# Kernel tuning notes

Hardware: AMD Instinct MI355X
Metric: run time of the kernel (lower is better)

The kernel has to match this reference:

```python
import jax, jax.numpy as jnp
import numpy as np

B, T, E, H, D = 1, 2048, 1024, 16, 64  # H*D == E required by module


def setup_inputs() -> dict:
    key = jax.random.key(0)
    ks = jax.random.split(key, 9)
    s_in = (2.0 / E) ** 0.5
    return {
        "x": jax.random.normal(ks[0], (B, T, E), jnp.float32),
        "wq": jax.random.normal(ks[1], (H * D, E), jnp.float32) * E ** -0.5,
        "wk": jax.random.normal(ks[2], (H * D, E), jnp.float32) * E ** -0.5,
        "wv": jax.random.normal(ks[3], (H * D, E), jnp.float32) * E ** -0.5,
        "wr": jax.random.normal(ks[4], (H, E, T), jnp.float32) * s_in,
        "wvr": jax.random.normal(ks[5], (H * D, E), jnp.float32) * E ** -0.5,
        "wj": jax.random.normal(ks[6], (E, E), jnp.float32) * E ** -0.5,
        "gate": jnp.zeros((H, 3), jnp.float32),
        "wo": jax.random.normal(ks[7], (E, H * D), jnp.float32) * E ** -0.5,
    }


def reference(x, wq, wk, wv, wr, wvr, wj, gate, wo):
    Bx, Tx, Ex = x.shape
    Hh = wr.shape[0]
    Dd = wq.shape[0] // Hh
    scale = 1.0 / Dd ** 0.5
    neg = -jnp.inf
    mask = jnp.triu(jnp.ones((Tx, Tx), bool), 1)  # True above diagonal

    def heads(w):  # (B,T,H*D) -> (B,H,T,D)
        return (x @ w.T).reshape(Bx, Tx, Hh, Dd).transpose(0, 2, 1, 3)

    # --- branch 1: standard causal QKV attention ---
    q, k, v = heads(wq), heads(wk), heads(wv)
    qkv_attn = jnp.einsum('bhqd,bhkd->bhqk', q, k) * scale
    qkv_attn = jnp.where(mask, neg, qkv_attn)
    qkv_out = jnp.einsum('bhqk,bhkd->bhqd', jax.nn.softmax(qkv_attn, axis=-1), v)

    # --- branch 2: RRPRAM learned per-position scores ---
    rv = heads(wvr)
    r = jnp.einsum('bte,het->bht', x, wr[:, :, :Tx])  # (B,H,T) key scores
    r_attn = jnp.where(mask, neg, (r * scale)[:, :, None, :])  # (B,H,T,T)
    rrp_out = jnp.einsum('bhqk,bhkd->bhqd', jax.nn.softmax(r_attn, axis=-1), rv)

    # --- branch 3: Janus self-resonance ---
    echo = x @ wj.T            # (B,T,E)
    echo_back = echo @ wj      # F.linear(echo, wj.weight.T)
    scores = (x * echo_back).sum(-1) / Ex ** 0.5  # (B,T)
    j_attn = jnp.where(mask, neg, scores[:, :, None] * scores[:, None, :])  # (B,T,T)
    jA = jax.nn.softmax(j_attn, axis=-1)
    j_val = echo.reshape(Bx, Tx, Hh, Dd).transpose(0, 2, 1, 3)
    jan_out = jnp.einsum('bqk,bhkd->bhqd', jA, j_val)

    # --- gated combine + output proj ---
    g = jax.nn.softmax(gate, axis=-1)  # (H,3)
    out = (g[:, 0][None, :, None, None] * qkv_out
           + g[:, 1][None, :, None, None] * rrp_out
           + g[:, 2][None, :, None, None] * jan_out)
    out = out.transpose(0, 2, 1, 3).reshape(Bx, Tx, Hh * Dd)
    return out @ wo.T
```

## Files before the change

kernel.cpp:

```cpp
#include <hip/hip_runtime.h>
#include <cstddef>
#include <cstdint>

#define TT 2048
#define EE 1024
#define HH 16

typedef unsigned short ushort;
typedef unsigned int uint;
typedef __attribute__((ext_vector_type(8))) short short8;
typedef __attribute__((ext_vector_type(8))) _Float16 half8;
typedef __attribute__((ext_vector_type(4))) float f32x4;
typedef __attribute__((ext_vector_type(4))) ushort ushort4v;

__device__ __forceinline__ ushort f2bf(float f) {
  uint u = __builtin_bit_cast(uint, f);
  u = (u + 0x7FFFu + ((u >> 16) & 1u)) >> 16;
  return (ushort)u;
}
__device__ __forceinline__ float bf2f(ushort h) {
  return __builtin_bit_cast(float, (uint)h << 16);
}
__device__ __forceinline__ ushort f2h(float f) {
  return __builtin_bit_cast(ushort, (_Float16)f);
}

__device__ __forceinline__ void async16(ushort* lds, const ushort* g) {
  __builtin_amdgcn_global_load_lds(
      reinterpret_cast<const __attribute__((address_space(1))) void*>(
          reinterpret_cast<uintptr_t>(g)),
      reinterpret_cast<__attribute__((address_space(3))) void*>(
          static_cast<unsigned int>(reinterpret_cast<uintptr_t>(lds))),
      16, 0, 0);
}

__global__ __launch_bounds__(256) void cvt_all(
    const float* __restrict__ x, ushort* __restrict__ xbf,
    ushort* __restrict__ xh, ushort* __restrict__ xTbf,
    const float* __restrict__ w0, const float* __restrict__ w1,
    const float* __restrict__ w2, const float* __restrict__ w3,
    const float* __restrict__ w4, const float* __restrict__ w5,
    ushort* __restrict__ d0, ushort* __restrict__ d1,
    ushort* __restrict__ d2, ushort* __restrict__ d3,
    ushort* __restrict__ d4, ushort* __restrict__ d5,
    float* __restrict__ snorm)
{
  const int z = blockIdx.z;
  if (z == 0) {
    __shared__ float tile[32][33];
    if (blockIdx.x == 0 && blockIdx.y == 0) {
      for (int i = threadIdx.x; i < TT; i += 256) snorm[i] = 0.f;
    }
    const int bn = blockIdx.x * 32;
    const int bm = blockIdx.y * 32;
    const int c4 = (threadIdx.x & 7) * 4;
    const int r  = threadIdx.x >> 3;
    const size_t off = (size_t)(bm + r) * EE + bn + c4;
    float4 v = *(const float4*)(x + off);
    tile[r][c4 + 0] = v.x; tile[r][c4 + 1] = v.y;
    tile[r][c4 + 2] = v.z; tile[r][c4 + 3] = v.w;
    ushort4v b, h;
    b.x = f2bf(v.x); b.y = f2bf(v.y); b.z = f2bf(v.z); b.w = f2bf(v.w);
    h.x = f2h(v.x);  h.y = f2h(v.y);  h.z = f2h(v.z);  h.w = f2h(v.w);
    *(ushort4v*)(xbf + off) = b;
    *(ushort4v*)(xh + off) = h;
    __syncthreads();
    const int t4 = (threadIdx.x & 7) * 4;
    const int e  = threadIdx.x >> 3;
    ushort4v tb;
    tb.x = f2bf(tile[t4 + 0][e]); tb.y = f2bf(tile[t4 + 1][e]);
    tb.z = f2bf(tile[t4 + 2][e]); tb.w = f2bf(tile[t4 + 3][e]);
    *(ushort4v*)(xTbf + (size_t)(bn + e) * TT + bm + t4) = tb;
    return;
  }
  const int lin = blockIdx.y * 32 + blockIdx.x;
  if (lin >= 1024) return;
  const float* src; ushort* dst;
  switch (z) {
    case 1: src = w0; dst = d0; break;
    case 2: src = w1; dst = d1; break;
    case 3: src = w2; dst = d2; break;
    case 4: src = w3; dst = d3; break;
    case 5: src = w4; dst = d4; break;
    default: src = w5; dst = d5; break;
  }
  const int i = lin * 1024 + threadIdx.x * 4;
  float4 v = *(const float4*)(src + i);
  ushort4v o;
  if (z == 6) {
    o.x = f2h(v.x); o.y = f2h(v.y); o.z = f2h(v.z); o.w = f2h(v.w);
  } else {
    o.x = f2bf(v.x); o.y = f2bf(v.y); o.z = f2bf(v.z); o.w = f2bf(v.w);
  }
  *(ushort4v*)(dst + i) = o;
}

__global__ __launch_bounds__(256) void proj5(
    const ushort* __restrict__ Abf, const ushort* __restrict__ Ah,
    const ushort* __restrict__ B0, const ushort* __restrict__ B1,
    const ushort* __restrict__ B2, const ushort* __restrict__ B3,
    const ushort* __restrict__ B4,
    ushort* __restrict__ C0, ushort* __restrict__ C1,
    ushort* __restrict__ C2, ushort* __restrict__ C3,
    ushort* __restrict__ C4, float* __restrict__ snorm,
    int M, int N, int K)
{
  const ushort* A; const ushort* B; ushort* C; int om;
  switch (blockIdx.z) {
    case 0: A = Abf; B = B0; C = C0; om = 1; break;
    case 1: A = Abf; B = B1; C = C1; om = 1; break;
    case 2: A = Abf; B = B2; C = C2; om = 2; break;
    case 3: A = Abf; B = B3; C = C3; om = 1; break;
    default: A = Ah; B = B4; C = C4; om = 3; break;
  }
  const bool f16 = (blockIdx.z == 4);
  __shared__ __align__(16) ushort As[2][128 * 64];
  __shared__ __align__(16) ushort Bs[2][128 * 64];
  const int tid = threadIdx.x;
  const int m0 = blockIdx.y * 128, n0 = blockIdx.x * 128;
  const int w = tid >> 6, lane = tid & 63;
  const int wr = w >> 1, wc = w & 1;
  const int lr = lane & 15, lk = lane >> 4;
  const int srow = lane >> 3;
  const int scol = ((lane & 7) ^ srow) * 8;
  const ushort* AgL = A + (size_t)(m0 + w * 32 + srow) * K + scol;
  const ushort* BgL = B + (size_t)(n0 + w * 32 + srow) * K + scol;
  const int sbase = (w * 32) * 64;
  const int s0 = (lk ^ (lr & 7)) * 8;
  f32x4 acc[4][4] = {};
  const int NT = K >> 6;
#pragma unroll
  for (int c = 0; c < 4; ++c) {
    async16(&As[0][sbase + c * 8 * 64], AgL + (size_t)c * 8 * K);
    async16(&Bs[0][sbase + c * 8 * 64], BgL + (size_t)c * 8 * K);
  }
  __syncthreads();
  for (int kt = 0; kt < NT; ++kt) {
    const int cur = kt & 1;
    if (kt + 1 < NT) {
      const int kn = (kt + 1) << 6;
#pragma unroll
      for (int c = 0; c < 4; ++c) {
        async16(&As[cur ^ 1][sbase + c * 8 * 64], AgL + (size_t)c * 8 * K + kn);
        async16(&Bs[cur ^ 1][sbase + c * 8 * 64], BgL + (size_t)c * 8 * K + kn);
      }
    }
    short8 a0[4], a1[4], b0[4], b1[4];
#pragma unroll
    for (int i = 0; i < 4; ++i) {
      const ushort* p = &As[cur][(wr * 64 + i * 16 + lr) * 64];
      a0[i] = *(const short8*)(p + s0);
      a1[i] = *(const short8*)(p + (s0 ^ 32));
    }
#pragma unroll
    for (int j = 0; j < 4; ++j) {
      const ushort* p = &Bs[cur][(wc * 64 + j * 16 + lr) * 64];
      b0[j] = *(const short8*)(p + s0);
      b1[j] = *(const short8*)(p + (s0 ^ 32));
    }
    if (f16) {
#pragma unroll
      for (int i = 0; i < 4; ++i)
#pragma unroll
        for (int j = 0; j < 4; ++j) {
          acc[i][j] = __builtin_amdgcn_mfma_f32_16x16x32_f16(
              __builtin_bit_cast(half8, a0[i]), __builtin_bit_cast(half8, b0[j]),
              acc[i][j], 0, 0, 0);
          acc[i][j] = __builtin_amdgcn_mfma_f32_16x16x32_f16(
              __builtin_bit_cast(half8, a1[i]), __builtin_bit_cast(half8, b1[j]),
              acc[i][j], 0, 0, 0);
        }
    } else {
#pragma unroll
      for (int i = 0; i < 4; ++i)
#pragma unroll
        for (int j = 0; j < 4; ++j) {
          acc[i][j] = __builtin_amdgcn_mfma_f32_16x16x32_bf16(
              a0[i], b0[j], acc[i][j], 0, 0, 0);
          acc[i][j] = __builtin_amdgcn_mfma_f32_16x16x32_bf16(
              a1[i], b1[j], acc[i][j], 0, 0, 0);
        }
    }
    __syncthreads();
  }
#pragma unroll
  for (int i = 0; i < 4; ++i)
#pragma unroll
    for (int r = 0; r < 4; ++r) {
      int row = m0 + wr * 64 + i * 16 + lk * 4 + r;
#pragma unroll
      for (int j = 0; j < 4; ++j) {
        int col = n0 + wc * 64 + j * 16 + lr;
        ushort v = (om == 2) ? f2h(acc[i][j][r]) : f2bf(acc[i][j][r]);
        if (om == 1)
          C[((size_t)(col >> 6) * M + row) * 64 + (col & 63)] = v;
        else if (om == 2)
          C[(size_t)(col >> 6) * 64 * M + (size_t)(col & 63) * M + row] = v;
        else
          C[(size_t)col * M + row] = v;
      }
    }
  if (om == 3) {
#pragma unroll
    for (int i = 0; i < 4; ++i)
#pragma unroll
      for (int r = 0; r < 4; ++r) {
        float p = 0.f;
#pragma unroll
        for (int j = 0; j < 4; ++j) p += acc[i][j][r] * acc[i][j][r];
        p += __shfl_xor(p, 1); p += __shfl_xor(p, 2);
        p += __shfl_xor(p, 4); p += __shfl_xor(p, 8);
        if (lr == 0)
          atomicAdd(&snorm[m0 + wr * 64 + i * 16 + lk * 4 + r], p);
      }
  }
}

template<bool CZ>
__global__ __launch_bounds__(256) void gemm_mfma(
    const ushort* __restrict__ A, const ushort* __restrict__ B,
    float* __restrict__ Cp, int M, int N, int K)
{
  __shared__ __align__(16) ushort As[2][128 * 64];
  __shared__ __align__(16) ushort Bs[2][128 * 64];
  const int tid = threadIdx.x;
  const int m0 = blockIdx.y * 128, n0 = blockIdx.x * 128;
  const int w = tid >> 6, lane = tid & 63;
  const int wr = w >> 1, wc = w & 1;
  const int lr = lane & 15, lk = lane >> 4;
  const int srow = lane >> 3;
  const int scol = ((lane & 7) ^ srow) * 8;
  const ushort* AgL = A + (size_t)(m0 + w * 32 + srow) * K + scol;
  const ushort* BgL = B + (size_t)(n0 + w * 32 + srow) * K + scol;
  const int sbase = (w * 32) * 64;
  const int s0 = (lk ^ (lr & 7)) * 8;
  f32x4 acc[4][4] = {};
  const int Keff = CZ ? (K < m0 + 128 ? K : m0 + 128) : K;
  const int NT = Keff >> 6;
#pragma unroll
  for (int c = 0; c < 4; ++c) {
    async16(&As[0][sbase + c * 8 * 64], AgL + (size_t)c * 8 * K);
    async16(&Bs[0][sbase + c * 8 * 64], BgL + (size_t)c * 8 * K);
  }
  __syncthreads();
  for (int kt = 0; kt < NT; ++kt) {
    const int cur = kt & 1;
    if (kt + 1 < NT) {
      const int kn = (kt + 1) << 6;
#pragma unroll
      for (int c = 0; c < 4; ++c) {
        async16(&As[cur ^ 1][sbase + c * 8 * 64], AgL + (size_t)c * 8 * K + kn);
        async16(&Bs[cur ^ 1][sbase + c * 8 * 64], BgL + (size_t)c * 8 * K + kn);
      }
    }
    short8 a0[4], a1[4], b0[4], b1[4];
#pragma unroll
    for (int i = 0; i < 4; ++i) {
      const ushort* p = &As[cur][(wr * 64 + i * 16 + lr) * 64];
      a0[i] = *(const short8*)(p + s0);
      a1[i] = *(const short8*)(p + (s0 ^ 32));
    }
#pragma unroll
    for (int j = 0; j < 4; ++j) {
      const ushort* p = &Bs[cur][(wc * 64 + j * 16 + lr) * 64];
      b0[j] = *(const short8*)(p + s0);
      b1[j] = *(const short8*)(p + (s0 ^ 32));
    }
#pragma unroll
    for (int i = 0; i < 4; ++i)
#pragma unroll
      for (int j = 0; j < 4; ++j) {
        acc[i][j] = __builtin_amdgcn_mfma_f32_16x16x32_bf16(
            a0[i], b0[j], acc[i][j], 0, 0, 0);
        acc[i][j] = __builtin_amdgcn_mfma_f32_16x16x32_bf16(
            a1[i], b1[j], acc[i][j], 0, 0, 0);
      }
    __syncthreads();
  }
#pragma unroll
  for (int i = 0; i < 4; ++i)
#pragma unroll
    for (int r = 0; r < 4; ++r) {
      int row = m0 + wr * 64 + i * 16 + lk * 4 + r;
#pragma unroll
      for (int j = 0; j < 4; ++j) {
        int col = n0 + wc * 64 + j * 16 + lr;
        Cp[(size_t)row * N + col] = acc[i][j][r];
      }
    }
}

__global__ __launch_bounds__(64) void flash_mfma(
    const ushort* __restrict__ Qg, const ushort* __restrict__ Kg,
    const ushort* __restrict__ Vg, ushort* __restrict__ O, int T, int nqt)
{
  const int bid = blockIdx.x;
  const int xcd = bid & 7;
  const int ii = bid >> 3;
  const int h = xcd * 2 + (ii & 1);
  const int w  = (ii >> 1) & 3;
  const int qt = (nqt - 1) - (ii >> 3);
  const int q0 = qt * 64;
  const int ke = qt + 1;
  const int lane = threadIdx.x & 63;
  const int lr = lane & 15, lk = lane >> 4;
  const ushort* Q = Qg + (size_t)h * T * 64;
  const ushort* K = Kg + (size_t)h * T * 64;
  const ushort* V = Vg + (size_t)h * 64 * T;
  __shared__ __align__(16) ushort Ps[16 * 72];
  const float CEXP = 0.18033688f;

  f32x4 o[4] = {};
  float ls[4] = {0.f, 0.f, 0.f, 0.f};

  short8 qa0 = *(const short8*)(Q + (size_t)(q0 + w * 16 + lr) * 64 + lk * 8);
  short8 qa1 = *(const short8*)(Q + (size_t)(q0 + w * 16 + lr) * 64 + 32 + lk * 8);
  short8 kb0[4], kb1[4];
#pragma unroll
  for (int c = 0; c < 4; ++c) {
    const ushort* kp = K + (size_t)(c * 16 + lr) * 64 + lk * 8;
    kb0[c] = *(const short8*)kp;
    kb1[c] = *(const short8*)(kp + 32);
  }
  for (int kt = 0; kt < ke; ++kt) {
    const int k0 = kt * 64;
    short8 vb0[4], vb1[4];
#pragma unroll
    for (int c = 0; c < 4; ++c) {
      const ushort* vp = V + (size_t)(c * 16 + lr) * T + k0 + lk * 8;
      vb0[c] = *(const short8*)vp;
      vb1[c] = *(const short8*)(vp + 32);
    }
    f32x4 s[4];
    __builtin_amdgcn_s_setprio(1);
#pragma unroll
    for (int c = 0; c < 4; ++c) {
      f32x4 z = {};
      z = __builtin_amdgcn_mfma_f32_16x16x32_bf16(qa0, kb0[c], z, 0, 0, 0);
      z = __builtin_amdgcn_mfma_f32_16x16x32_bf16(qa1, kb1[c], z, 0, 0, 0);
      s[c] = z;
    }
    __builtin_amdgcn_s_setprio(0);
    if (kt + 1 < ke) {
#pragma unroll
      for (int c = 0; c < 4; ++c) {
        const ushort* kp = K + (size_t)(k0 + 64 + c * 16 + lr) * 64 + lk * 8;
        kb0[c] = *(const short8*)kp;
        kb1[c] = *(const short8*)(kp + 32);
      }
    }
    float pv[4][4];
#pragma unroll
    for (int c = 0; c < 4; ++c)
#pragma unroll
      for (int r = 0; r < 4; ++r)
        pv[c][r] = exp2f(s[c][r] * CEXP);
    if (kt == qt) {
      const int rowbase = q0 + w * 16 + lk * 4;
#pragma unroll
      for (int c = 0; c < 4; ++c) {
        const int col = k0 + c * 16 + lr;
#pragma unroll
        for (int r = 0; r < 4; ++r)
          if (col > rowbase + r) pv[c][r] = 0.f;
      }
    }
#pragma unroll
    for (int c = 0; c < 4; ++c)
#pragma unroll
      for (int r = 0; r < 4; ++r) {
        ls[r] += pv[c][r];
        Ps[(lk * 4 + r) * 72 + c * 16 + lr] = f2h(pv[c][r]);
      }
    short8 pa0 = *(const short8*)(&Ps[lr * 72 + lk * 8]);
    short8 pa1 = *(const short8*)(&Ps[lr * 72 + 32 + lk * 8]);
    __builtin_amdgcn_s_setprio(1);
#pragma unroll
    for (int c = 0; c < 4; ++c) {
      o[c] = __builtin_amdgcn_mfma_f32_16x16x32_f16(
          __builtin_bit_cast(half8, pa0), __builtin_bit_cast(half8, vb0[c]),
          o[c], 0, 0, 0);
      o[c] = __builtin_amdgcn_mfma_f32_16x16x32_f16(
          __builtin_bit_cast(half8, pa1), __builtin_bit_cast(half8, vb1[c]),
          o[c], 0, 0, 0);
    }
    __builtin_amdgcn_s_setprio(0);
  }
#pragma unroll
  for (int r = 0; r < 4; ++r) {
    ls[r] += __shfl_xor(ls[r], 1);
    ls[r] += __shfl_xor(ls[r], 2);
    ls[r] += __shfl_xor(ls[r], 4);
    ls[r] += __shfl_xor(ls[r], 8);
    ls[r] = 1.f / ls[r];
  }
  ushort* Oh = O + ((size_t)h * T + q0) * 64;
#pragma unroll
  for (int c = 0; c < 4; ++c)
#pragma unroll
    for (int r = 0; r < 4; ++r) {
      int row = w * 16 + lk * 4 + r;
      Oh[(size_t)row * 64 + c * 16 + lr] = f2bf(o[c][r] * ls[r]);
    }
}

__global__ __launch_bounds__(256) void combine_kernel(
    const ushort* __restrict__ a1, const ushort* __restrict__ a2,
    const float* __restrict__ jraw, const float* __restrict__ denj,
    const float* __restrict__ gate, ushort* __restrict__ comb, int T)
{
  const int idx = blockIdx.x * 256 + threadIdx.x;
  const int t = idx >> 10;
  const int c = idx & 1023;
  const int h = c >> 6;
  const int d = c & 63;
  float g0 = gate[h * 3 + 0], g1 = gate[h * 3 + 1], g2 = gate[h * 3 + 2];
  float mg = fmaxf(g0, fmaxf(g1, g2));
  float e0 = __expf(g0 - mg), e1 = __expf(g1 - mg), e2 = __expf(g2 - mg);
  float inv = 1.f / (e0 + e1 + e2);
  const size_t hd = ((size_t)h * T + t) * 64 + d;
  float v = (e0 * bf2f(a1[hd]) + e1 * bf2f(a2[hd]) + e2 * jraw[idx] / denj[t]) * inv;
  comb[idx] = f2bf(v);
}

__global__ __launch_bounds__(256) void rscore6(
    const ushort* __restrict__ xTbf, const float* __restrict__ wr,
    float* __restrict__ rpart, int T, int E)
{
  const int h = blockIdx.y;
  const int e0 = blockIdx.z * 64;
  const int t0 = (blockIdx.x * 256 + threadIdx.x) * 4;
  const float* wrh = wr + (size_t)h * E * T;
  float4 acc = {0.f, 0.f, 0.f, 0.f};
#pragma unroll 4
  for (int e = e0; e < e0 + 64; ++e) {
    ushort4v xv = *(const ushort4v*)(xTbf + (size_t)e * T + t0);
    float4 wv = *(const float4*)(wrh + (size_t)e * T + t0);
    acc.x += bf2f(xv.x) * wv.x;
    acc.y += bf2f(xv.y) * wv.y;
    acc.z += bf2f(xv.z) * wv.z;
    acc.w += bf2f(xv.w) * wv.w;
  }
  *(float4*)(rpart + ((size_t)blockIdx.z * HH + h) * T + t0) = acc;
}

__global__ __launch_bounds__(256) void jw_rsm(
    const float* __restrict__ snorm, ushort* __restrict__ Wb,
    float* __restrict__ den, const float* __restrict__ rpart,
    float* __restrict__ wwb, int T)
{
  __shared__ float rs[TT];
  __shared__ float red[4];
  if ((int)blockIdx.x < T) {
    const int q = blockIdx.x;
    const float sq = snorm[q] * 0.03125f;
    float mx = -1e30f;
    for (int k = threadIdx.x; k <= q; k += 256)
      mx = fmaxf(mx, sq * (snorm[k] * 0.03125f));
#pragma unroll
    for (int o = 32; o; o >>= 1) mx = fmaxf(mx, __shfl_xor(mx, o));
    if ((threadIdx.x & 63) == 0) red[threadIdx.x >> 6] = mx;
    __syncthreads();
    mx = fmaxf(fmaxf(red[0], red[1]), fmaxf(red[2], red[3]));
    float sum = 0.f;
    ushort* Wq = Wb + (size_t)q * T;
    for (int k = threadIdx.x; k < T; k += 256) {
      float wv = (k <= q) ? __expf(sq * (snorm[k] * 0.03125f) - mx) : 0.f;
      ushort wb = f2bf(wv);
      Wq[k] = wb;
      sum += bf2f(wb);
    }
#pragma unroll
    for (int o = 32; o; o >>= 1) sum += __shfl_xor(sum, o);
    __syncthreads();
    if ((threadIdx.x & 63) == 0) red[threadIdx.x >> 6] = sum;
    __syncthreads();
    if (threadIdx.x == 0) den[q] = red[0] + red[1] + red[2] + red[3];
  } else {
    const int h = blockIdx.x - T;
    for (int t = threadIdx.x; t < T; t += 256) {
      float a = 0.f;
#pragma unroll
      for (int s = 0; s < 16; ++s) a += rpart[((size_t)s * HH + h) * T + t];
      rs[t] = a;
    }
    __syncthreads();
    float mx = -1e30f;
    for (int t = threadIdx.x; t < T; t += 256) mx = fmaxf(mx, rs[t]);
#pragma unroll
    for (int o = 32; o; o >>= 1) mx = fmaxf(mx, __shfl_xor(mx, o));
    if ((threadIdx.x & 63) == 0) red[threadIdx.x >> 6] = mx;
    __syncthreads();
    mx = fmaxf(fmaxf(red[0], red[1]), fmaxf(red[2], red[3]));
    float* wh = wwb + (size_t)h * T;
    for (int t = threadIdx.x; t < T; t += 256)
      wh[t] = __expf((rs[t] - mx) * 0.125f);
  }
}

__global__ __launch_bounds__(64) void rrp_part(
    const float* __restrict__ wgt, const ushort* __restrict__ rv,
    float* __restrict__ segsum, int T)
{
  const int h = blockIdx.x, seg = blockIdx.y, d = threadIdx.x;
  const int segLen = T >> 5;
  const int kbeg = seg * segLen;
  __shared__ __align__(16) ushort rvs[64 * 64];
  __shared__ float wls[64];
  wls[d] = wgt[(size_t)h * T + kbeg + d];
  {
    const short8* src = (const short8*)(rv + (size_t)h * T * 64 +
                                        (size_t)kbeg * 64);
    short8* dst = (short8*)rvs;
#pragma unroll
    for (int j = 0; j < 8; ++j) dst[j * 64 + d] = src[j * 64 + d];
  }
  __syncthreads();
  float num = 0.f, den = 0.f;
  for (int k = 0; k < segLen; ++k) {
    float wk = wls[k];
    num += wk * bf2f(rvs[k * 64 + d]);
    den += wk;
  }
  float* o = segsum + ((size_t)h * 32 + seg) * 65;
  o[d] = num;
  if (d == 0) o[64] = den;
}

__global__ __launch_bounds__(64) void rrp_scan2(
    const float* __restrict__ wgt, const ushort* __restrict__ rv,
    const float* __restrict__ segsum, ushort* __restrict__ out, int T)
{
  const int h = blockIdx.x, seg = blockIdx.y, d = threadIdx.x;
  const int segLen = T >> 5;
  const int kbeg = seg * segLen;
  __shared__ __align__(16) ushort rvs[64 * 64];
  __shared__ float wls[64];
  wls[d] = wgt[(size_t)h * T + kbeg + d];
  {
    const short8* src = (const short8*)(rv + (size_t)h * T * 64 +
                                        (size_t)kbeg * 64);
    short8* dst = (short8*)rvs;
#pragma unroll
    for (int j = 0; j < 8; ++j) dst[j * 64 + d] = src[j * 64 + d];
  }
  float num = 0.f, den = 0.f;
  for (int s = 0; s < seg; ++s) {
    const float* p = segsum + ((size_t)h * 32 + s) * 65;
    num += p[d];
    den += p[64];
  }
  __syncthreads();
  for (int k = 0; k < segLen; ++k) {
    float wk = wls[k];
    num += wk * bf2f(rvs[k * 64 + d]);
    den += wk;
    rvs[k * 64 + d] = f2bf(num / den);
  }
  __syncthreads();
  {
    short8* dst = (short8*)(out + (size_t)h * T * 64 + (size_t)kbeg * 64);
    const short8* src = (const short8*)rvs;
#pragma unroll
    for (int j = 0; j < 8; ++j) dst[j * 64 + d] = src[j * 64 + d];
  }
}

extern "C" void kernel_launch(void* const* d_in, const int* in_sizes, int n_in,
                              void* d_out, int out_size, void* d_ws, size_t ws_size,
                              hipStream_t stream)
{
  (void)in_sizes; (void)n_in; (void)out_size; (void)ws_size;
  const float* x    = (const float*)d_in[0];
  const float* wq   = (const float*)d_in[1];
  const float* wk   = (const float*)d_in[2];
  const float* wv   = (const float*)d_in[3];
  const float* wr   = (const float*)d_in[4];
  const float* wvr  = (const float*)d_in[5];
  const float* wj   = (const float*)d_in[6];
  const float* gate = (const float*)d_in[7];
  const float* wo   = (const float*)d_in[8];
  float* out = (float*)d_out;

  const int T = TT, E = EE, H = HH;
  const int nqt = T / 64;
  const size_t TE = (size_t)T * E;
  const size_t EE2 = (size_t)E * E;
  const size_t TT2 = (size_t)T * T;

  ushort* u = (ushort*)d_ws;
  ushort* xbf   = u;
  ushort* xh    = xbf + TE;
  ushort* xTbf  = xh + TE;
  ushort* wqb   = xTbf + TE;
  ushort* wkb   = wqb + EE2;
  ushort* wvb   = wkb + EE2;
  ushort* wvrb  = wvb + EE2;
  ushort* wob   = wvrb + EE2;
  ushort* wjh   = wob + EE2;
  ushort* qhb   = wjh + EE2;
  ushort* khb   = qhb + TE;
  ushort* vtb   = khb + TE;
  ushort* rvhb  = vtb + TE;
  ushort* echoT = rvhb + TE;
  ushort* a1b   = echoT + TE;
  ushort* a2b   = a1b + TE;
  ushort* Wbf   = a2b + TE;
  ushort* combb = Wbf + TT2;
  float* jraw   = (float*)(combb + TE);
  float* wwb    = jraw + TE;
  float* snorm  = wwb + (size_t)H * T;
  float* denj   = snorm + T;
  float* rpart  = denj + T;
  float* segsum = rpart + (size_t)16 * H * T;

  dim3 blk(256);
  cvt_all<<<dim3(E / 32, T / 32, 7), blk, 0, stream>>>(
      x, xbf, xh, xTbf, wq, wk, wv, wvr, wo, wj,
      wqb, wkb, wvb, wvrb, wob, wjh, snorm);

  proj5<<<dim3(E / 128, T / 128, 5), blk, 0, stream>>>(
      xbf, xh, wqb, wkb, wvb, wvrb, wjh,
      qhb, khb, vtb, rvhb, echoT, snorm, T, E, E);

  rscore6<<<dim3(T / 1024, H, E / 64), blk, 0, stream>>>(
      xTbf, wr, rpart, T, E);

  jw_rsm<<<T + H, blk, 0, stream>>>(snorm, Wbf, denj, rpart, wwb, T);

  flash_mfma<<<dim3(H * nqt * 4), dim3(64), 0, stream>>>(
      qhb, khb, vtb, a1b, T, nqt);

  rrp_part<<<dim3(H, 32), dim3(64), 0, stream>>>(wwb, rvhb, segsum, T);
  rrp_scan2<<<dim3(H, 32), dim3(64), 0, stream>>>(wwb, rvhb, segsum, a2b, T);

  gemm_mfma<true><<<dim3(E / 128, T / 128), blk, 0, stream>>>(
      Wbf, echoT, jraw, T, E, T);

  combine_kernel<<<(int)(TE / 256), blk, 0, stream>>>(a1b, a2b, jraw, denj,
                                                      gate, combb, T);
  gemm_mfma<false><<<dim3(E / 128, T / 128), blk, 0, stream>>>(
      combb, wob, (float*)out, T, E, E);
}
```

Measured before the change: 416.2 us.

## Fuse gated combine into Janus GEMM epilogue and merge rrp_part into flash launch

```diff
diff --git a/kernel.cpp b/kernel.cpp
--- a/kernel.cpp
+++ b/kernel.cpp
@@ -216,8 +216,7 @@
   }
 }
 
-template<bool CZ>
-__global__ __launch_bounds__(256) void gemm_mfma(
+__global__ __launch_bounds__(256) void gemm_out(
     const ushort* __restrict__ A, const ushort* __restrict__ B,
     float* __restrict__ Cp, int M, int N, int K)
 {
@@ -235,8 +234,7 @@
   const int sbase = (w * 32) * 64;
   const int s0 = (lk ^ (lr & 7)) * 8;
   f32x4 acc[4][4] = {};
-  const int Keff = CZ ? (K < m0 + 128 ? K : m0 + 128) : K;
-  const int NT = Keff >> 6;
+  const int NT = K >> 6;
 #pragma unroll
   for (int c = 0; c < 4; ++c) {
     async16(&As[0][sbase + c * 8 * 64], AgL + (size_t)c * 8 * K);
@@ -290,10 +288,125 @@
     }
 }
 
-__global__ __launch_bounds__(64) void flash_mfma(
+__global__ __launch_bounds__(256) void gemm_janus(
+    const ushort* __restrict__ A, const ushort* __restrict__ B,
+    const ushort* __restrict__ a1b, const ushort* __restrict__ a2b,
+    const float* __restrict__ denj, const float* __restrict__ gate,
+    ushort* __restrict__ comb, int M, int N, int K)
+{
+  __shared__ __align__(16) ushort As[2][128 * 64];
+  __shared__ __align__(16) ushort Bs[2][128 * 64];
+  const int tid = threadIdx.x;
+  const int m0 = blockIdx.y * 128, n0 = blockIdx.x * 128;
+  const int w = tid >> 6, lane = tid & 63;
+  const int wr = w >> 1, wc = w & 1;
+  const int lr = lane & 15, lk = lane >> 4;
+  const int srow = lane >> 3;
+  const int scol = ((lane & 7) ^ srow) * 8;
+  const ushort* AgL = A + (size_t)(m0 + w * 32 + srow) * K + scol;
+  const ushort* BgL = B + (size_t)(n0 + w * 32 + srow) * K + scol;
+  const int sbase = (w * 32) * 64;
+  const int s0 = (lk ^ (lr & 7)) * 8;
+  f32x4 acc[4][4] = {};
+  const int Keff = (K < m0 + 128) ? K : (m0 + 128);
+  const int NT = Keff >> 6;
+#pragma unroll
+  for (int c = 0; c < 4; ++c) {
+    async16(&As[0][sbase + c * 8 * 64], AgL + (size_t)c * 8 * K);
+    async16(&Bs[0][sbase + c * 8 * 64], BgL + (size_t)c * 8 * K);
+  }
+  __syncthreads();
+  for (int kt = 0; kt < NT; ++kt) {
+    const int cur = kt & 1;
+    if (kt + 1 < NT) {
+      const int kn = (kt + 1) << 6;
+#pragma unroll
+      for (int c = 0; c < 4; ++c) {
+        async16(&As[cur ^ 1][sbase + c * 8 * 64], AgL + (size_t)c * 8 * K + kn);
+        async16(&Bs[cur ^ 1][sbase + c * 8 * 64], BgL + (size_t)c * 8 * K + kn);
+      }
+    }
+    short8 a0[4], a1[4], b0[4], b1[4];
+#pragma unroll
+    for (int i = 0; i < 4; ++i) {
+      const ushort* p = &As[cur][(wr * 64 + i * 16 + lr) * 64];
+      a0[i] = *(const short8*)(p + s0);
+      a1[i] = *(const short8*)(p + (s0 ^ 32));
+    }
+#pragma unroll
+    for (int j = 0; j < 4; ++j) {
+      const ushort* p = &Bs[cur][(wc * 64 + j * 16 + lr) * 64];
+      b0[j] = *(const short8*)(p + s0);
+      b1[j] = *(const short8*)(p + (s0 ^ 32));
+    }
+#pragma unroll
+    for (int i = 0; i < 4; ++i)
+#pragma unroll
+      for (int j = 0; j < 4; ++j) {
+        acc[i][j] = __builtin_amdgcn_mfma_f32_16x16x32_bf16(
+            a0[i], b0[j], acc[i][j], 0, 0, 0);
+        acc[i][j] = __builtin_amdgcn_mfma_f32_16x16x32_bf16(
+            a1[i], b1[j], acc[i][j], 0, 0, 0);
+      }
+    __syncthreads();
+  }
+  const int hA = blockIdx.x * 2 + wc;
+  const float g0 = gate[hA * 3 + 0], g1 = gate[hA * 3 + 1],
+              g2 = gate[hA * 3 + 2];
+  const float mg = fmaxf(g0, fmaxf(g1, g2));
+  const float e0 = __expf(g0 - mg), e1 = __expf(g1 - mg),
+              e2 = __expf(g2 - mg);
+  const float inv = 1.f / (e0 + e1 + e2);
+#pragma unroll
+  for (int i = 0; i < 4; ++i)
+#pragma unroll
+    for (int r = 0; r < 4; ++r) {
+      const int row = m0 + wr * 64 + i * 16 + lk * 4 + r;
+      const float dj = e2 / denj[row];
+#pragma unroll
+      for (int j = 0; j < 4; ++j) {
+        const int d = j * 16 + lr;
+        const size_t hd = ((size_t)hA * M + row) * 64 + d;
+        const float v =
+            (e0 * bf2f(a1b[hd]) + e1 * bf2f(a2b[hd]) + dj * acc[i][j][r]) * inv;
+        comb[(size_t)row * N + n0 + wc * 64 + d] = f2bf(v);
+      }
+    }
+}
+
+__global__ __launch_bounds__(64) void flash_rrp(
     const ushort* __restrict__ Qg, const ushort* __restrict__ Kg,
-    const ushort* __restrict__ Vg, ushort* __restrict__ O, int T, int nqt)
-{
+    const ushort* __restrict__ Vg, ushort* __restrict__ O,
+    const float* __restrict__ wgt, const ushort* __restrict__ rv,
+    float* __restrict__ segsum, int T, int nqt, int NF)
+{
+  __shared__ __align__(16) ushort sbuf[64 * 64];
+  __shared__ float wls[64];
+  if ((int)blockIdx.x >= NF) {
+    const int bid = blockIdx.x - NF;
+    const int h = bid >> 5, seg = bid & 31, d = threadIdx.x;
+    const int segLen = T >> 5;
+    const int kbeg = seg * segLen;
+    wls[d] = wgt[(size_t)h * T + kbeg + d];
+    {
+      const short8* src = (const short8*)(rv + (size_t)h * T * 64 +
+                                          (size_t)kbeg * 64);
+      short8* dst = (short8*)sbuf;
+#pragma unroll
+      for (int j = 0; j < 8; ++j) dst[j * 64 + d] = src[j * 64 + d];
+    }
+    __syncthreads();
+    float num = 0.f, den = 0.f;
+    for (int k = 0; k < segLen; ++k) {
+      float wk = wls[k];
+      num += wk * bf2f(sbuf[k * 64 + d]);
+      den += wk;
+    }
+    float* o = segsum + ((size_t)h * 32 + seg) * 65;
+    o[d] = num;
+    if (d == 0) o[64] = den;
+    return;
+  }
   const int bid = blockIdx.x;
   const int xcd = bid & 7;
   const int ii = bid >> 3;
@@ -307,7 +420,7 @@
   const ushort* Q = Qg + (size_t)h * T * 64;
   const ushort* K = Kg + (size_t)h * T * 64;
   const ushort* V = Vg + (size_t)h * 64 * T;
-  __shared__ __align__(16) ushort Ps[16 * 72];
+  ushort* Ps = sbuf;
   const float CEXP = 0.18033688f;
 
   f32x4 o[4] = {};
@@ -402,25 +515,6 @@
       int row = w * 16 + lk * 4 + r;
       Oh[(size_t)row * 64 + c * 16 + lr] = f2bf(o[c][r] * ls[r]);
     }
-}
-
-__global__ __launch_bounds__(256) void combine_kernel(
-    const ushort* __restrict__ a1, const ushort* __restrict__ a2,
-    const float* __restrict__ jraw, const float* __restrict__ denj,
-    const float* __restrict__ gate, ushort* __restrict__ comb, int T)
-{
-  const int idx = blockIdx.x * 256 + threadIdx.x;
-  const int t = idx >> 10;
-  const int c = idx & 1023;
-  const int h = c >> 6;
-  const int d = c & 63;
-  float g0 = gate[h * 3 + 0], g1 = gate[h * 3 + 1], g2 = gate[h * 3 + 2];
-  float mg = fmaxf(g0, fmaxf(g1, g2));
-  float e0 = __expf(g0 - mg), e1 = __expf(g1 - mg), e2 = __expf(g2 - mg);
-  float inv = 1.f / (e0 + e1 + e2);
-  const size_t hd = ((size_t)h * T + t) * 64 + d;
-  float v = (e0 * bf2f(a1[hd]) + e1 * bf2f(a2[hd]) + e2 * jraw[idx] / denj[t]) * inv;
-  comb[idx] = f2bf(v);
 }
 
 __global__ __launch_bounds__(256) void rscore6(
@@ -496,35 +590,6 @@
     for (int t = threadIdx.x; t < T; t += 256)
       wh[t] = __expf((rs[t] - mx) * 0.125f);
   }
-}
-
-__global__ __launch_bounds__(64) void rrp_part(
-    const float* __restrict__ wgt, const ushort* __restrict__ rv,
-    float* __restrict__ segsum, int T)
-{
-  const int h = blockIdx.x, seg = blockIdx.y, d = threadIdx.x;
-  const int segLen = T >> 5;
-  const int kbeg = seg * segLen;
-  __shared__ __align__(16) ushort rvs[64 * 64];
-  __shared__ float wls[64];
-  wls[d] = wgt[(size_t)h * T + kbeg + d];
-  {
-    const short8* src = (const short8*)(rv + (size_t)h * T * 64 +
-                                        (size_t)kbeg * 64);
-    short8* dst = (short8*)rvs;
-#pragma unroll
-    for (int j = 0; j < 8; ++j) dst[j * 64 + d] = src[j * 64 + d];
-  }
-  __syncthreads();
-  float num = 0.f, den = 0.f;
-  for (int k = 0; k < segLen; ++k) {
-    float wk = wls[k];
-    num += wk * bf2f(rvs[k * 64 + d]);
-    den += wk;
-  }
-  float* o = segsum + ((size_t)h * 32 + seg) * 65;
-  o[d] = num;
-  if (d == 0) o[64] = den;
 }
 
 __global__ __launch_bounds__(64) void rrp_scan2(
@@ -607,8 +672,7 @@
   ushort* a2b   = a1b + TE;
   ushort* Wbf   = a2b + TE;
   ushort* combb = Wbf + TT2;
-  float* jraw   = (float*)(combb + TE);
-  float* wwb    = jraw + TE;
+  float* wwb    = (float*)(combb + TE);
   float* snorm  = wwb + (size_t)H * T;
   float* denj   = snorm + T;
   float* rpart  = denj + T;
@@ -628,17 +692,15 @@
 
   jw_rsm<<<T + H, blk, 0, stream>>>(snorm, Wbf, denj, rpart, wwb, T);
 
-  flash_mfma<<<dim3(H * nqt * 4), dim3(64), 0, stream>>>(
-      qhb, khb, vtb, a1b, T, nqt);
-
-  rrp_part<<<dim3(H, 32), dim3(64), 0, stream>>>(wwb, rvhb, segsum, T);
+  const int NF = H * nqt * 4;
+  flash_rrp<<<dim3(NF + H * 32), dim3(64), 0, stream>>>(
+      qhb, khb, vtb, a1b, wwb, rvhb, segsum, T, nqt, NF);
+
   rrp_scan2<<<dim3(H, 32), dim3(64), 0, stream>>>(wwb, rvhb, segsum, a2b, T);
 
-  gemm_mfma<true><<<dim3(E / 128, T / 128), blk, 0, stream>>>(
-      Wbf, echoT, jraw, T, E, T);
-
-  combine_kernel<<<(int)(TE / 256), blk, 0, stream>>>(a1b, a2b, jraw, denj,
-                                                      gate, combb, T);
-  gemm_mfma<false><<<dim3(E / 128, T / 128), blk, 0, stream>>>(
+  gemm_janus<<<dim3(E / 128, T / 128), blk, 0, stream>>>(
+      Wbf, echoT, a1b, a2b, denj, gate, combb, T, E, T);
+
+  gemm_out<<<dim3(E / 128, T / 128), blk, 0, stream>>>(
       combb, wob, (float*)out, T, E, E);
 }
```

Result: faster. 407.6 us (median of 2 runs) (-2.1%).
